# Optimization experiments

Hardware: AMD Instinct MI355X
Metric: run time of the kernel (lower is better)

## Reference

```python
import jax, jax.numpy as jnp
import numpy as np

B, T, D, H = 2, 4096, 1024, 16
DK, DV, C = 64, 128, 64  # head_k_dim, head_v_dim, chunk size


def setup_inputs() -> dict:
    key = jax.random.key(0)
    ks = jax.random.split(key, 7)
    std = 0.02
    return {
        "x": jax.random.normal(ks[0], (B, T, D), jnp.float32),
        "Wq": jax.random.normal(ks[1], (D, D), jnp.float32) * std,
        "Wk": jax.random.normal(ks[2], (D, D), jnp.float32) * std,
        "Wv": jax.random.normal(ks[3], (D, 2 * D), jnp.float32) * std,
        "Wg": jax.random.normal(ks[4], (D, 2 * D), jnp.float32) * std,
        "Wo": jax.random.normal(ks[5], (2 * D, D), jnp.float32) * std,
        "g_norm_w": jnp.ones((DV,), jnp.float32),
    }


def _rope(q, k):  # q,k: [B,T,H,DK], neox-style rotate-half rotary
    dk = q.shape[-1]
    inv = 1.0 / (10000.0 ** (jnp.arange(0, dk, 2, dtype=jnp.float32) / dk))
    t = jnp.arange(q.shape[1], dtype=jnp.float32)
    f = t[:, None] * inv[None, :]                      # [T, dk/2]
    cos = jnp.cos(f)[None, :, None, :]
    sin = jnp.sin(f)[None, :, None, :]
    def rot(x):
        x1, x2 = jnp.split(x, 2, axis=-1)
        return jnp.concatenate([x1 * cos - x2 * sin, x1 * sin + x2 * cos], -1)
    return rot(q), rot(k)


def reference(x, Wq, Wk, Wv, Wg, Wo, g_norm_w):
    b, t, _ = x.shape
    nc = t // C
    q = (x @ Wq).reshape(b, t, H, DK)
    k = (x @ Wk).reshape(b, t, H, DK)
    v = (x @ Wv).reshape(b, t, H, DV)
    g = (x @ Wg).reshape(b, t, H, DV)
    q, k = _rope(q, k)
    q = q * (DK ** -0.5)

    # per-head retention decay: gamma_h = 1 - 2^(-5-h)
    gamma = 1.0 - jnp.exp2(-5.0 - jnp.arange(H, dtype=jnp.float32))  # [H]
    i = jnp.arange(C, dtype=jnp.float32)
    dq = gamma[:, None] ** (i + 1.0)          # [H,C] cross-chunk decay on q
    dkv = gamma[:, None] ** (C - 1.0 - i)     # [H,C] decay of k into state
    rel = i[:, None] - i[None, :]
    Dmat = jnp.where(rel >= 0, gamma[:, None, None] ** jnp.maximum(rel, 0.0), 0.0)  # [H,C,C]
    gC = gamma ** C

    to_chunks = lambda a: a.reshape(b, nc, C, H, a.shape[-1]).transpose(1, 0, 3, 2, 4)
    qc, kc, vc = to_chunks(q), to_chunks(k), to_chunks(v)  # [NC,B,H,C,d]

    def step(S, inp):
        qi, ki, vi = inp
        o_inter = jnp.einsum('bhcd,bhde->bhce', qi * dq[None, :, :, None], S)
        A = jnp.einsum('bhid,bhjd->bhij', qi, ki) * Dmat[None]
        o_intra = jnp.einsum('bhij,bhje->bhie', A, vi)
        S = gC[None, :, None, None] * S + jnp.einsum('bhjd,bhje->bhde', ki * dkv[None, :, :, None], vi)
        return S, o_inter + o_intra

    S0 = jnp.zeros((b, H, DK, DV), x.dtype)
    _, o = jax.lax.scan(step, S0, (qc, kc, vc))            # [NC,B,H,C,DV]
    o = o.transpose(1, 0, 3, 2, 4).reshape(b, t, H, DV)

    # fused per-head RMSNorm + swish gate
    rms = o * jax.lax.rsqrt(jnp.mean(o * o, axis=-1, keepdims=True) + 1e-5) * g_norm_w
    o = rms * (g * jax.nn.sigmoid(g))
    return o.reshape(b, t, H * DV) @ Wo
```

## Files before the change

kernel.cpp:

```cpp
#include <hip/hip_runtime.h>
#include <stdint.h>
#include <type_traits>

typedef unsigned short u16;
typedef __attribute__((ext_vector_type(8))) short short8;
typedef __attribute__((ext_vector_type(4))) float f32x4;

#define MFMA16(a,b,c) __builtin_amdgcn_mfma_f32_16x16x32_bf16(a,b,c,0,0,0)

__device__ __forceinline__ u16 f2bf(float f){
  uint32_t u = __builtin_bit_cast(uint32_t, f);
  u += 0x7FFFu + ((u>>16)&1u);
  return (u16)(u>>16);
}
__device__ __forceinline__ float bf2f(u16 h){
  uint32_t u = ((uint32_t)h)<<16;
  return __builtin_bit_cast(float, u);
}

__global__ __launch_bounds__(256) void prep(const float* __restrict__ x, u16* __restrict__ xb,
    const float* __restrict__ Wq, const float* __restrict__ Wk, const float* __restrict__ Wv,
    const float* __restrict__ Wg, const float* __restrict__ Wo,
    u16* __restrict__ WcatT, u16* __restrict__ WoT){
  int bid = blockIdx.x;
  if (bid < 8192){
    int i = (bid*256 + threadIdx.x)*4;
    float4 v = *(const float4*)&x[i];
    uint2 u;
    u.x = (uint32_t)f2bf(v.x) | ((uint32_t)f2bf(v.y)<<16);
    u.y = (uint32_t)f2bf(v.z) | ((uint32_t)f2bf(v.w)<<16);
    *(uint2*)&xb[i] = u;
    return;
  }
  bid -= 8192;
  const float* src; u16* dst; int R, Cc, tc, tr;
  if (bid < 1024){        src=Wq; dst=WcatT;             R=1024; Cc=1024; int b=bid;      tc=(b&31)*32; tr=(b>>5)*32; }
  else if (bid < 2048){   src=Wk; dst=WcatT+1024*1024;   R=1024; Cc=1024; int b=bid-1024; tc=(b&31)*32; tr=(b>>5)*32; }
  else if (bid < 4096){   src=Wv; dst=WcatT+2048*1024;   R=1024; Cc=2048; int b=bid-2048; tc=(b&63)*32; tr=(b>>6)*32; }
  else if (bid < 6144){   src=Wg; dst=WcatT+4096*1024;   R=1024; Cc=2048; int b=bid-4096; tc=(b&63)*32; tr=(b>>6)*32; }
  else {                  src=Wo; dst=WoT;               R=2048; Cc=1024; int b=bid-6144; tc=(b&31)*32; tr=(b>>5)*32; }
  __shared__ float tile[32][33];
  int lr = threadIdx.x>>5, lc = threadIdx.x&31;
  #pragma unroll
  for (int p=0;p<4;p++)
    tile[lr+p*8][lc] = src[(size_t)(tr+lr+p*8)*Cc + tc + lc];
  __syncthreads();
  #pragma unroll
  for (int p=0;p<4;p++)
    dst[(size_t)(tc+lr+p*8)*R + tr + lc] = f2bf(tile[lc][lr+p*8]);
}

__global__ __launch_bounds__(512,1) void gemm1_256(const u16* __restrict__ A,
    const u16* __restrict__ BT, u16* __restrict__ C){
  __shared__ u16 L[4*16384];
  const int flat = blockIdx.y*24 + blockIdx.x;
  const int xcd  = flat & 7, loc = flat >> 3;
  const int bm   = xcd*4 + (loc & 3);
  const int bn   = loc >> 2;
  const int t = threadIdx.x;
  const int w = t>>6, l = t&63;
  const int wm = w>>2, wn = w&3;
  const int lr = l&15, lg = l>>4;
  const int srow = t>>2;
  const int gsw = ((t&3) - (t>>3)) & 3;
  const size_t aoff = (size_t)(bm*256 + srow)*1024 + gsw*8;
  const size_t boff = (size_t)(bn*256 + srow)*1024 + gsw*8;
  const int sdo = t*8;

  u16 *p0 = L, *p1 = L+16384, *p2 = L+32768, *p3 = L+49152;

  auto STAGE = [&](u16* buf, int k0){
    __builtin_amdgcn_global_load_lds(&A[aoff + k0],                     buf + sdo,               16,0,0);
    __builtin_amdgcn_global_load_lds(&A[aoff + (size_t)128*1024 + k0],  buf + sdo + 4096,        16,0,0);
    __builtin_amdgcn_global_load_lds(&BT[boff + k0],                    buf + 8192 + sdo,        16,0,0);
    __builtin_amdgcn_global_load_lds(&BT[boff + (size_t)128*1024 + k0], buf + 8192 + sdo + 4096, 16,0,0);
  };

  f32x4 acc[8][4];
  #pragma unroll
  for (int m=0;m<8;m++)
    #pragma unroll
    for (int n=0;n<4;n++) acc[m][n] = (f32x4){0.f,0.f,0.f,0.f};

  STAGE(p0, 0); STAGE(p1, 32); STAGE(p2, 64);
  for (int kt=0; kt<32; ++kt){
    if      (kt < 30) asm volatile("s_waitcnt vmcnt(8)" ::: "memory");
    else if (kt == 30) asm volatile("s_waitcnt vmcnt(4)" ::: "memory");
    else               asm volatile("s_waitcnt vmcnt(0)" ::: "memory");
    __builtin_amdgcn_s_barrier();
    if (kt+3 < 32) STAGE(p3, (kt+3)*32);
    short8 af[8], bf4[4];
    #pragma unroll
    for (int m=0;m<8;m++){
      int row = wm*128 + m*16 + lr;
      af[m] = *(const short8*)(p0 + row*32 + (((lg + (row>>1))&3)<<3));
    }
    #pragma unroll
    for (int n=0;n<4;n++){
      int row = wn*64 + n*16 + lr;
      bf4[n] = *(const short8*)(p0 + 8192 + row*32 + (((lg + (row>>1))&3)<<3));
    }
    __builtin_amdgcn_s_setprio(1);
    #pragma unroll
    for (int m=0;m<8;m++)
      #pragma unroll
      for (int n=0;n<4;n++)
        acc[m][n] = MFMA16(af[m], bf4[n], acc[m][n]);
    __builtin_amdgcn_s_setprio(0);
    { u16* tp=p0; p0=p1; p1=p2; p2=p3; p3=tp; }
  }

  __syncthreads();
  const bool qk = (bn < 8);
  const float qscale = (bn < 4) ? 0.125f : 1.0f;
  #pragma unroll
  for (int s=0;s<4;++s){
    if (wm == (s>>1)){
      #pragma unroll
      for (int mm=0;mm<4;++mm){
        const int m = (s&1)*4 + mm;
        if (qk){
          #pragma unroll
          for (int n=0;n<2;n++){
            float inv = exp2f((float)(n*16+lr) * (-13.287712379549449f/32.0f));
            #pragma unroll
            for (int r=0;r<4;r++){
              int grow = bm*256 + wm*128 + m*16 + lg*4 + r;
              float f = (float)(grow & 4095) * inv;
              float sn, cs; __sincosf(f, &sn, &cs);
              float x1 = acc[m][n][r], x2 = acc[m][n+2][r];
              int lrow = mm*16 + lg*4 + r;
              L[lrow*264 + wn*64 + n*16 + lr]     = f2bf((x1*cs - x2*sn)*qscale);
              L[lrow*264 + wn*64 + (n+2)*16 + lr] = f2bf((x1*sn + x2*cs)*qscale);
            }
          }
        } else {
          #pragma unroll
          for (int n=0;n<4;n++)
            #pragma unroll
            for (int r=0;r<4;r++)
              L[(mm*16+lg*4+r)*264 + wn*64 + n*16 + lr] = f2bf(acc[m][n][r]);
        }
      }
    }
    __syncthreads();
    #pragma unroll
    for (int p=0;p<4;p++){
      int idx = p*512 + t;
      int row = idx>>5, gr = idx&31;
      *(short8*)&C[(size_t)(bm*256 + s*64 + row)*6144 + bn*256 + gr*8] =
        *(const short8*)&L[row*264 + gr*8];
    }
    __syncthreads();
  }
}

__global__ __launch_bounds__(256) void gemm2_nt(const u16* __restrict__ A,
    const u16* __restrict__ BT, float* __restrict__ C, int M, int N, int K){
  __shared__ u16 L[3*8192];
  const int flat = blockIdx.y*gridDim.x + blockIdx.x;
  const int xcd  = flat & 7, loc = flat >> 3;
  const int bm   = xcd*8 + (loc & 7);
  const int bn   = loc >> 3;
  const int t = threadIdx.x;
  const int w = t>>6, l = t&63;
  const int wr = (w>>1)*64, wc = (w&1)*64;
  const int lr = l&15, lg = l>>4;
  const int srow = t>>2;
  const int gsw  = ((t&3) - (t>>3)) & 3;
  const int scol = gsw*8;
  const size_t aoff = (size_t)(bm*128 + srow)*K + scol;
  const size_t boff = (size_t)(bn*128 + srow)*K + scol;
  const int sdo = t*8;

  u16 *a0 = L,          *b0 = L + 4096;
  u16 *a1 = L + 8192,   *b1 = L + 12288;
  u16 *a2 = L + 16384,  *b2 = L + 20480;

  auto STAGE = [&](u16* la, u16* lb, int k0){
    __builtin_amdgcn_global_load_lds(&A[aoff + k0],                 la + sdo,        16, 0, 0);
    __builtin_amdgcn_global_load_lds(&A[aoff + (size_t)64*K + k0],  la + sdo + 2048, 16, 0, 0);
    __builtin_amdgcn_global_load_lds(&BT[boff + k0],                lb + sdo,        16, 0, 0);
    __builtin_amdgcn_global_load_lds(&BT[boff + (size_t)64*K + k0], lb + sdo + 2048, 16, 0, 0);
  };

  f32x4 acc[4][4];
  for (int m=0;m<4;m++) for (int n=0;n<4;n++) acc[m][n] = (f32x4){0.f,0.f,0.f,0.f};

  const int NT = K >> 5;
  STAGE(a0, b0, 0);
  STAGE(a1, b1, 32);
  for (int kt=0; kt<NT; ++kt){
    if (kt < NT-1) asm volatile("s_waitcnt vmcnt(4)" ::: "memory");
    else           asm volatile("s_waitcnt vmcnt(0)" ::: "memory");
    __builtin_amdgcn_s_barrier();
    if (kt+2 < NT) STAGE(a2, b2, (kt+2)*32);
    short8 af[4], bfr[4];
    #pragma unroll
    for (int m=0;m<4;m++){
      int rrow = wr + m*16 + lr;
      af[m]  = *(const short8*)(a0 + rrow*32 + (((lg + (rrow>>1))&3)<<3));
    }
    #pragma unroll
    for (int n=0;n<4;n++){
      int rrow = wc + n*16 + lr;
      bfr[n] = *(const short8*)(b0 + rrow*32 + (((lg + (rrow>>1))&3)<<3));
    }
    __builtin_amdgcn_s_setprio(1);
    #pragma unroll
    for (int m=0;m<4;m++)
      #pragma unroll
      for (int n=0;n<4;n++)
        acc[m][n] = MFMA16(af[m], bfr[n], acc[m][n]);
    __builtin_amdgcn_s_setprio(0);
    { u16* tp=a0; a0=a1; a1=a2; a2=tp; }
    { u16* tp=b0; b0=b1; b1=b2; b2=tp; }
  }

  #pragma unroll
  for (int m=0;m<4;m++)
    #pragma unroll
    for (int n=0;n<4;n++){
    int row = bm*128 + wr + m*16 + lg*4;
    int col = bn*128 + wc + n*16 + lr;
    #pragma unroll
    for (int r=0;r<4;r++)
      C[(size_t)(row+r)*N + col] = acc[m][n][r];
  }
}

__global__ __launch_bounds__(256) void retention_r1(const u16* __restrict__ qkvg,
    u16* __restrict__ o, u16* __restrict__ states){
  int bid = blockIdx.x;
  int c = bid & 63, h = (bid>>6)&15, b = bid>>10;
  int t = threadIdx.x, w = t>>6, l = t&63, lr = l&15, lg = l>>4;
  __shared__ u16 SH[17280];
  __shared__ float pw[72];
  u16* kT    = SH;
  u16* vT    = SH + 4096;
  u16* A_lds = SH + 12288;
  float log2g = log2f(1.0f - exp2f(-5.0f - (float)h));
  if (t < 65) pw[t] = exp2f(log2g*(float)t);
  const size_t rowbase = (size_t)(b*4096 + c*64);
  __syncthreads();

  {
    int rp = t>>3, cg = t&7;
    int r0 = rp*2;
    short8 k0v = *(const short8*)&qkvg[(rowbase+r0  )*6144 + 1024 + h*64 + cg*8];
    short8 k1v = *(const short8*)&qkvg[(rowbase+r0+1)*6144 + 1024 + h*64 + cg*8];
    float d0 = pw[63-r0], d1 = pw[62-r0];
    #pragma unroll
    for (int j=0;j<8;j++){
      int d = cg*8+j;
      uint32_t pk = (uint32_t)f2bf(bf2f((u16)k0v[j])*d0) | ((uint32_t)f2bf(bf2f((u16)k1v[j])*d1)<<16);
      *(uint32_t*)&kT[d*64 + (((r0>>3) ^ (d>>3))<<3) + (r0&7)] = pk;
    }
    #pragma unroll
    for (int p=0;p<2;p++){
      int it = t + p*256;
      int vrp = it>>4, vcg = it&15;
      int vr0 = vrp*2;
      short8 v0 = *(const short8*)&qkvg[(rowbase+vr0  )*6144 + 2048 + h*128 + vcg*8];
      short8 v1 = *(const short8*)&qkvg[(rowbase+vr0+1)*6144 + 2048 + h*128 + vcg*8];
      #pragma unroll
      for (int j=0;j<8;j++){
        int e = vcg*8+j;
        uint32_t pv = (uint32_t)(u16)v0[j] | ((uint32_t)(u16)v1[j]<<16);
        *(uint32_t*)&vT[e*64 + (((vr0>>3) ^ ((e>>3)&7))<<3) + (vr0&7)] = pv;
      }
    }
  }

  f32x4 z4 = {0.f,0.f,0.f,0.f};
  f32x4 accA[4] = {z4,z4,z4,z4};
  #pragma unroll
  for (int ks=0;ks<2;ks++){
    short8 aq = *(const short8*)&qkvg[(rowbase + w*16+lr)*6144 + h*64 + ks*32 + lg*8];
    #pragma unroll
    for (int n=0;n<4;n++){
      short8 bk = *(const short8*)&qkvg[(rowbase + n*16+lr)*6144 + 1024 + h*64 + ks*32 + lg*8];
      accA[n] = MFMA16(aq, bk, accA[n]);
    }
  }
  #pragma unroll
  for (int n=0;n<4;n++)
    #pragma unroll
    for (int r=0;r<4;r++){
    int i = w*16 + lg*4 + r, j = n*16 + lr;
    float v = (i>=j) ? accA[n][r]*pw[i-j] : 0.0f;
    A_lds[i*72 + j] = f2bf(v);
  }
  __syncthreads();

  f32x4 accO[8], accS[8];
  #pragma unroll
  for (int n=0;n<8;n++){ accO[n]=z4; accS[n]=z4; }
  #pragma unroll
  for (int ks=0;ks<2;ks++){
    int rk = w*16+lr;
    short8 aA = *(const short8*)&A_lds[rk*72 + ks*32+lg*8];
    short8 aK = *(const short8*)&kT[rk*64 + (((ks*4+lg) ^ (rk>>3))<<3)];
    #pragma unroll
    for (int n=0;n<8;n++){
      int e2 = n*16+lr;
      short8 bv = *(const short8*)&vT[e2*64 + (((ks*4+lg) ^ ((e2>>3)&7))<<3)];
      accO[n] = MFMA16(aA, bv, accO[n]);
      accS[n] = MFMA16(aK, bv, accS[n]);
    }
  }

  __syncthreads();
  u16* oB = SH;
  u16* sB = SH + 8448;
  #pragma unroll
  for (int n=0;n<8;n++)
    #pragma unroll
    for (int r=0;r<4;r++){
    int i = w*16 + lg*4 + r, e = n*16 + lr;
    oB[i*132 + e] = f2bf(accO[n][r]);
    sB[e*68 + i]  = f2bf(accS[n][r]);
  }
  __syncthreads();
  const size_t ob = rowbase*2048 + h*128;
  const size_t sb = ((size_t)(b*16+h)*64 + c)*8192;
  {
    int orow = t>>2, ocol = (t&3)*32;
    #pragma unroll
    for (int q=0;q<4;q++)
      *(short8*)&o[ob + (size_t)orow*2048 + ocol + q*8] = *(const short8*)&oB[orow*132 + ocol + q*8];
    int se = t>>1, sd = (t&1)*32;
    #pragma unroll
    for (int q=0;q<4;q++)
      *(short8*)&states[sb + (size_t)se*64 + sd + q*8] = *(const short8*)&sB[se*68 + sd + q*8];
  }
}

__global__ __launch_bounds__(256) void retention_r2(const u16* __restrict__ qkvg,
    const u16* __restrict__ states, u16* __restrict__ o){
  int bid = blockIdx.x;
  int vblk = bid & 7, h = (bid>>3)&15, b = bid>>7;
  int t = threadIdx.x, w = t>>6, l = t&63, lr = l&15, lg = l>>4;
  int e0 = vblk*16;
  float log2g = log2f(1.0f - exp2f(-5.0f - (float)h));
  float gC = exp2f(64.0f*log2g);
  float dqv[4];
  #pragma unroll
  for (int r=0;r<4;r++) dqv[r] = exp2f(log2g*(float)(w*16 + lg*4 + r + 1));
  float st[16];
  #pragma unroll
  for (int i=0;i<16;i++) st[i]=0.f;
  const size_t sbase = ((size_t)(b*16+h)*64)*8192 + (size_t)(e0+lr)*64 + lg*8;
  const size_t qb = (size_t)(b*4096)*6144 + h*64 + (size_t)(w*16+lr)*6144 + lg*8;
  const size_t obh = (size_t)(b*4096)*2048 + h*128 + e0 + lr;
  short8 nsc0 = *(const short8*)&states[sbase];
  short8 nsc1 = *(const short8*)&states[sbase + 32];
  short8 naq0 = *(const short8*)&qkvg[qb];
  short8 naq1 = *(const short8*)&qkvg[qb + 32];
  for (int c=0;c<64;c++){
    short8 sc0 = nsc0, sc1 = nsc1, aq0 = naq0, aq1 = naq1;
    if (c < 63){
      nsc0 = *(const short8*)&states[sbase + (size_t)(c+1)*8192];
      nsc1 = *(const short8*)&states[sbase + (size_t)(c+1)*8192 + 32];
      naq0 = *(const short8*)&qkvg[qb + (size_t)(c+1)*64*6144];
      naq1 = *(const short8*)&qkvg[qb + (size_t)(c+1)*64*6144 + 32];
    }
    f32x4 acc = {0.f,0.f,0.f,0.f};
    short8 bs0, bs1;
    #pragma unroll
    for (int dd=0;dd<8;dd++) bs0[dd] = (short)f2bf(st[dd]);
    #pragma unroll
    for (int dd=0;dd<8;dd++) bs1[dd] = (short)f2bf(st[dd+8]);
    acc = MFMA16(aq0, bs0, acc);
    acc = MFMA16(aq1, bs1, acc);
    #pragma unroll
    for (int r=0;r<4;r++){
      int i = w*16 + lg*4 + r;
      size_t oi = obh + (size_t)(c*64 + i)*2048;
      o[oi] = f2bf(bf2f(o[oi]) + dqv[r]*acc[r]);
    }
    #pragma unroll
    for (int i2=0;i2<8;i2++) st[i2]   = gC*st[i2]   + bf2f((u16)sc0[i2]);
    #pragma unroll
    for (int i2=0;i2<8;i2++) st[i2+8] = gC*st[i2+8] + bf2f((u16)sc1[i2]);
  }
}

__global__ __launch_bounds__(256) void norm_gate(const u16* __restrict__ o,
    const u16* __restrict__ qkvg, const float* __restrict__ gnw, u16* __restrict__ og){
  int g16 = threadIdx.x >> 4;
  int l16 = threadIdx.x & 15;
  int rowh = blockIdx.x*16 + g16;
  int row = rowh >> 4, h = rowh & 15;
  short8 vv = *(const short8*)(o + (size_t)row*2048 + h*128 + l16*8);
  float v[8];
  float ss = 0.f;
  #pragma unroll
  for (int j=0;j<8;j++){ v[j] = bf2f((u16)vv[j]); ss += v[j]*v[j]; }
  #pragma unroll
  for (int off=8; off; off>>=1) ss += __shfl_xor(ss, off);
  float rs = rsqrtf(ss*(1.0f/128.0f) + 1e-5f);
  short8 gg = *(const short8*)(qkvg + (size_t)row*6144 + 4096 + h*128 + l16*8);
  float4 w0 = *(const float4*)&gnw[l16*8];
  float4 w1 = *(const float4*)&gnw[l16*8 + 4];
  float wv[8] = {w0.x,w0.y,w0.z,w0.w,w1.x,w1.y,w1.z,w1.w};
  short8 res;
  #pragma unroll
  for (int j=0;j<8;j++){
    float gj = bf2f((u16)gg[j]);
    float rj = v[j]*rs*wv[j] * (gj/(1.f+expf(-gj)));
    res[j] = (short)f2bf(rj);
  }
  *(short8*)(og + (size_t)row*2048 + h*128 + l16*8) = res;
}

extern "C" void kernel_launch(void* const* d_in, const int* in_sizes, int n_in,
                              void* d_out, int out_size, void* d_ws, size_t ws_size,
                              hipStream_t stream){
  const float* x   = (const float*)d_in[0];
  const float* Wq  = (const float*)d_in[1];
  const float* Wk  = (const float*)d_in[2];
  const float* Wv  = (const float*)d_in[3];
  const float* Wg  = (const float*)d_in[4];
  const float* Wo  = (const float*)d_in[5];
  const float* gnw = (const float*)d_in[6];
  float* out = (float*)d_out;

  const size_t NEED = 171966464ull;
  if (ws_size < NEED) return;

  char* base = (char*)d_ws;
  u16* qkvg  = (u16*)(base);
  u16* obuf  = (u16*)(base + 100663296);
  u16* WoT   = (u16*)(base + 134217728);
  u16* xb    = (u16*)(base + 138412032);
  u16* WcatT = (u16*)(base + 155189248);
  u16* stt   = (u16*)(base + 138412032);
  u16* og    = (u16*)(base + 138412032);

  prep<<<16384,256,0,stream>>>(x, xb, Wq, Wk, Wv, Wg, Wo, WcatT, WoT);
  gemm1_256<<<dim3(24,32),512,0,stream>>>(xb, WcatT, qkvg);
  retention_r1<<<2048,256,0,stream>>>(qkvg, obuf, stt);
  retention_r2<<<256,256,0,stream>>>(qkvg, stt, obuf);
  norm_gate<<<8192,256,0,stream>>>(obuf, qkvg, gnw, og);
  gemm2_nt<<<dim3(8,64),256,0,stream>>>(og, WoT, out, 8192, 1024, 2048);
}
```

Before: 292.9 us.

## Software-pipeline LDS fragment loads across MFMA halves in projection GEMM

Splits each k-step's 8x4 MFMA block into two halves and overlaps the LDS reads for the second A half, and for the next stage's A and B fragments, with the MFMAs of the other half. The barrier and vmcnt wait move to the middle of the iteration, so the next buffer's fragments can be prefetched while the current stage still computes. This aims to hide LDS read latency behind MFMA work in the main GEMM, at the cost of extra registers (double-buffered B fragments) and tighter wait-count bookkeeping.

Result: no change. 287.6 us (-1.8%).

```diff
diff --git a/kernel.cpp b/kernel.cpp
--- a/kernel.cpp
+++ b/kernel.cpp
@@ -75,6 +75,9 @@
     __builtin_amdgcn_global_load_lds(&BT[boff + k0],                    buf + 8192 + sdo,        16,0,0);
     __builtin_amdgcn_global_load_lds(&BT[boff + (size_t)128*1024 + k0], buf + 8192 + sdo + 4096, 16,0,0);
   };
+  auto LDA = [&](const u16* base, int row)->short8 {
+    return *(const short8*)(base + row*32 + (((lg + (row>>1))&3)<<3));
+  };
 
   f32x4 acc[8][4];
   #pragma unroll
@@ -83,30 +86,49 @@
     for (int n=0;n<4;n++) acc[m][n] = (f32x4){0.f,0.f,0.f,0.f};
 
   STAGE(p0, 0); STAGE(p1, 32); STAGE(p2, 64);
+  asm volatile("s_waitcnt vmcnt(8)" ::: "memory");
+  __builtin_amdgcn_s_barrier();
+  short8 afA[4], afB[4], bf4[4], bf4n[4];
+  #pragma unroll
+  for (int m=0;m<4;m++) afA[m] = LDA(p0, wm*128 + m*16 + lr);
+  #pragma unroll
+  for (int n=0;n<4;n++) bf4[n] = LDA(p0 + 8192, wn*64 + n*16 + lr);
+
   for (int kt=0; kt<32; ++kt){
-    if      (kt < 30) asm volatile("s_waitcnt vmcnt(8)" ::: "memory");
-    else if (kt == 30) asm volatile("s_waitcnt vmcnt(4)" ::: "memory");
+    #pragma unroll
+    for (int m=0;m<4;m++) afB[m] = LDA(p0, wm*128 + (m+4)*16 + lr);
+    if (kt+3 < 32) STAGE(p3, (kt+3)*32);
+    __builtin_amdgcn_s_setprio(1);
+    #pragma unroll
+    for (int m=0;m<4;m++)
+      #pragma unroll
+      for (int n=0;n<4;n++)
+        acc[m][n] = MFMA16(afA[m], bf4[n], acc[m][n]);
+    __builtin_amdgcn_s_setprio(0);
+    asm volatile("s_waitcnt lgkmcnt(0)" ::: "memory");
+    __builtin_amdgcn_sched_barrier(0);
+    if      (kt < 29)  asm volatile("s_waitcnt vmcnt(8)" ::: "memory");
+    else if (kt == 29) asm volatile("s_waitcnt vmcnt(4)" ::: "memory");
     else               asm volatile("s_waitcnt vmcnt(0)" ::: "memory");
     __builtin_amdgcn_s_barrier();
-    if (kt+3 < 32) STAGE(p3, (kt+3)*32);
-    short8 af[8], bf4[4];
-    #pragma unroll
-    for (int m=0;m<8;m++){
-      int row = wm*128 + m*16 + lr;
-      af[m] = *(const short8*)(p0 + row*32 + (((lg + (row>>1))&3)<<3));
-    }
-    #pragma unroll
-    for (int n=0;n<4;n++){
-      int row = wn*64 + n*16 + lr;
-      bf4[n] = *(const short8*)(p0 + 8192 + row*32 + (((lg + (row>>1))&3)<<3));
+    __builtin_amdgcn_sched_barrier(0);
+    if (kt+1 < 32){
+      #pragma unroll
+      for (int m=0;m<4;m++) afA[m]  = LDA(p1, wm*128 + m*16 + lr);
+      #pragma unroll
+      for (int n=0;n<4;n++) bf4n[n] = LDA(p1 + 8192, wn*64 + n*16 + lr);
     }
     __builtin_amdgcn_s_setprio(1);
     #pragma unroll
-    for (int m=0;m<8;m++)
+    for (int m=0;m<4;m++)
       #pragma unroll
       for (int n=0;n<4;n++)
-        acc[m][n] = MFMA16(af[m], bf4[n], acc[m][n]);
+        acc[m+4][n] = MFMA16(afB[m], bf4[n], acc[m+4][n]);
     __builtin_amdgcn_s_setprio(0);
+    if (kt+1 < 32){
+      #pragma unroll
+      for (int n=0;n<4;n++) bf4[n] = bf4n[n];
+    }
     { u16* tp=p0; p0=p1; p1=p2; p2=p3; p3=tp; }
   }
 
```
